# Optimization experiments

Hardware: AMD Instinct MI355X
Metric: run time of the kernel (lower is better)

The kernel has to match this reference:

```python
import jax, jax.numpy as jnp
import numpy as np

B = 512            # num graphs
NPG = 128          # nodes per graph (== output_dim; required by masked_fill broadcast)
N = B * NPG        # 65536 total nodes
EPG = 1024         # edges per graph
E = B * EPG        # 524288 edges
IN_D, HID_D, OUT_D = 128, 128, 128
EPS = 1e-5         # BatchNorm1d default eps
NEG = -10000000000.0


def setup_inputs() -> dict:
    key = jax.random.key(0)
    k = jax.random.split(key, 16)
    x = jax.random.normal(k[0], (N, IN_D), dtype=jnp.float32)
    # intra-graph random edges (PyG Batch never has cross-graph edges)
    g = jnp.repeat(jnp.arange(B, dtype=jnp.int32), EPG)
    src = g * NPG + jax.random.randint(k[1], (E,), 0, NPG, dtype=jnp.int32)
    dst = g * NPG + jax.random.randint(k[2], (E,), 0, NPG, dtype=jnp.int32)
    edge_index = jnp.stack([src, dst])  # [2, E]
    batch = jnp.repeat(jnp.arange(B, dtype=jnp.int32), NPG)  # [N]

    def lin(kk, fi, fo):
        s = 1.0 / np.sqrt(fi)
        return jax.random.uniform(kk, (fi, fo), jnp.float32, -s, s)

    W1 = lin(k[3], IN_D, HID_D); b1 = jnp.zeros((HID_D,), jnp.float32)
    W2 = lin(k[4], HID_D, HID_D); b2 = jnp.zeros((HID_D,), jnp.float32)
    W3 = lin(k[5], HID_D, OUT_D); b3 = jnp.zeros((OUT_D,), jnp.float32)
    gamma1 = jnp.ones((HID_D,), jnp.float32); beta1 = jnp.zeros((HID_D,), jnp.float32)
    gamma2 = jnp.ones((HID_D,), jnp.float32); beta2 = jnp.zeros((HID_D,), jnp.float32)
    rm1 = 0.1 * jax.random.normal(k[6], (HID_D,), jnp.float32)
    rv1 = jax.random.uniform(k[7], (HID_D,), jnp.float32, 0.5, 1.5)
    rm2 = 0.1 * jax.random.normal(k[8], (HID_D,), jnp.float32)
    rv2 = jax.random.uniform(k[9], (HID_D,), jnp.float32, 0.5, 1.5)
    return dict(x=x, edge_index=edge_index, batch=batch,
                W1=W1, b1=b1, gamma1=gamma1, beta1=beta1, rm1=rm1, rv1=rv1,
                W2=W2, b2=b2, gamma2=gamma2, beta2=beta2, rm2=rm2, rv2=rv2,
                W3=W3, b3=b3)


def reference(x, edge_index, batch, W1, b1, gamma1, beta1, rm1, rv1,
              W2, b2, gamma2, beta2, rm2, rv2, W3, b3):
    src, dst = edge_index[0], edge_index[1]
    loops = jnp.arange(N, dtype=src.dtype)
    fs = jnp.concatenate([src, loops])  # sources with self-loops
    fd = jnp.concatenate([dst, loops])  # targets with self-loops
    deg = jax.ops.segment_sum(jnp.ones_like(fd, jnp.float32), fd, num_segments=N)
    dis = jnp.where(deg > 0, jax.lax.rsqrt(deg), 0.0)
    norm = dis[fs] * dis[fd]  # D^-1/2 A_hat D^-1/2 per edge

    def gcn(h, W, b):
        h = h @ W
        msg = h[fs] * norm[:, None]            # [E+N, d] gather
        return jax.ops.segment_sum(msg, fd, num_segments=N) + b  # scatter-add

    def bn(h, g, bt, rm, rv):  # BatchNorm1d in eval mode (running stats)
        return (h - rm) * jax.lax.rsqrt(rv + EPS) * g + bt

    h = jax.nn.relu(bn(gcn(x, W1, b1), gamma1, beta1, rm1, rv1))
    # dropout is a no-op in eval mode
    h = jax.nn.relu(bn(gcn(h, W2, b2), gamma2, beta2, rm2, rv2))
    h = gcn(h, W3, b3)

    # global mean pool (all graphs have exactly NPG nodes)
    pooled = jax.ops.segment_sum(h, batch, num_segments=B) / NPG  # [B, OUT_D]

    # vectorized get_visited_nodes_and_update_embeddings:
    # a node is 'connected' if it appears as src or dst of an edge of its graph;
    # the minimum connected node index of each graph is exempted.
    connected = jnp.zeros((N,), bool).at[src].set(True).at[dst].set(True)
    ids = jnp.arange(N, dtype=jnp.int32)
    cand = jnp.where(connected, ids, N)
    min_pg = jax.ops.segment_min(cand, batch, num_segments=B)  # [B]
    mask = connected & (ids != min_pg[batch])                  # [N]
    return jnp.where(mask.reshape(B, NPG), NEG, pooled)
```

## Files before the change

### kernel.cpp

```cpp
#include <hip/hip_runtime.h>
#include <hip/hip_bf16.h>


#define NGRAPH 512
#define EPG 1024
#define NEDGE (NGRAPH * EPG)
#define NEGV -10000000000.0f
#define LDS_MAIN 62468

typedef float f32x16 __attribute__((ext_vector_type(16)));
typedef float f32x4  __attribute__((ext_vector_type(4)));

#define MFMA8(a, b, c) __builtin_amdgcn_mfma_f32_32x32x16_fp8_fp8(a, b, c, 0, 0, 0)

__device__ unsigned char g_wf[32768];

__device__ __forceinline__ unsigned swz8(unsigned row, unsigned byte_in_row) {
  return ((row << 7) + byte_in_row) ^ ((row & 15u) << 3);
}

__device__ __forceinline__ unsigned pk4(float a, float b, float c, float d) {
  int r = __builtin_amdgcn_cvt_pk_fp8_f32(a, b, 0, false);
  r = __builtin_amdgcn_cvt_pk_fp8_f32(c, d, r, true);
  return (unsigned)r;
}

__global__ void prep_w(const float* __restrict__ W1, const float* __restrict__ W2) {
  int gid = blockIdx.x * 256 + threadIdx.x;
  int lyr = gid >> 11, r = gid & 2047;
  int lane = r & 63, ks = (r >> 6) & 7, nt = r >> 9;
  const float* W = lyr ? W2 : W1;
  int fo = nt * 32 + (lane & 31);
  int k0 = ks * 16 + (lane >> 5) * 8;
  uint2 o;
  o.x = pk4(W[(k0 + 0) * 128 + fo], W[(k0 + 1) * 128 + fo],
            W[(k0 + 2) * 128 + fo], W[(k0 + 3) * 128 + fo]);
  o.y = pk4(W[(k0 + 4) * 128 + fo], W[(k0 + 5) * 128 + fo],
            W[(k0 + 6) * 128 + fo], W[(k0 + 7) * 128 + fo]);
  ((uint2*)g_wf)[gid] = o;
}

__global__ __launch_bounds__(512, 4) void gcn_all(
    const float* __restrict__ x, const int* __restrict__ ei,
    const float* __restrict__ b1v, const float* __restrict__ g1v,
    const float* __restrict__ be1v, const float* __restrict__ rm1v,
    const float* __restrict__ rv1v,
    const float* __restrict__ b2v, const float* __restrict__ g2v,
    const float* __restrict__ be2v, const float* __restrict__ rm2v,
    const float* __restrict__ rv2v,
    const float* __restrict__ W3g, const float* __restrict__ b3v,
    float* __restrict__ out) {
  extern __shared__ char sm[];
  char* AnB = sm;
  char* Y0  = sm + 16384;
  char* X0  = sm + 32768;
  unsigned* cntW  = (unsigned*)(sm + 49152);
  float*    dis   = (float*)(sm + 57344);
  unsigned* deg   = (unsigned*)(sm + 57856);
  unsigned* conn  = (unsigned*)(sm + 58368);
  float*    csumE = (float*)(sm + 58880);
  float*    scl1  = (float*)(sm + 59392);
  float*    shf1  = (float*)(sm + 59904);
  float*    scl2  = (float*)(sm + 60416);
  float*    shf2  = (float*)(sm + 60928);
  float*    vred  = (float*)(sm + 61440);
  int*      minid = (int*)(sm + 62464);

  const int tid = threadIdx.x;
  const int g   = blockIdx.x;
  const int lane = tid & 63;
  const int wid  = tid >> 6;
  const int l31  = lane & 31;
  const int hi   = lane >> 5;
  const int mt   = wid >> 1;
  const int nt0  = (wid & 1) * 2;

  const f32x4* xg = (const f32x4*)(x + (size_t)g * 128 * 128);
  f32x4 xr[8];
#pragma unroll
  for (int j = 0; j < 8; ++j) xr[j] = xg[tid + 512 * j];
  int es[2], ed[2];
#pragma unroll
  for (int j = 0; j < 2; ++j) {
    int e = g * EPG + tid + 512 * j;
    es[j] = ei[e] & 127;
    ed[j] = ei[NEDGE + e] & 127;
  }
  long wb0[8], wb1[8];
#pragma unroll
  for (int ks = 0; ks < 8; ++ks) {
    wb0[ks] = *(const long*)(g_wf + (nt0 + 0) * 4096 + ks * 512 + lane * 8);
    wb1[ks] = *(const long*)(g_wf + (nt0 + 1) * 4096 + ks * 512 + lane * 8);
  }

  {
    uint4 z; z.x = 0; z.y = 0; z.z = 0; z.w = 0;
    ((uint4*)cntW)[tid] = z;
  }
  if (tid < 128) {
    deg[tid] = 1u; conn[tid] = 0u; csumE[tid] = 0.f; vred[tid] = 0.f;
    float s1 = rsqrtf(rv1v[tid] + 1e-5f) * g1v[tid];
    scl1[tid] = s1;
    shf1[tid] = be1v[tid] + (b1v[tid] - rm1v[tid]) * s1;
    float s2 = rsqrtf(rv2v[tid] + 1e-5f) * g2v[tid];
    scl2[tid] = s2;
    shf2[tid] = be2v[tid] + (b2v[tid] - rm2v[tid]) * s2;
  }
  if (tid == 0) *minid = 128;
  __syncthreads();

#pragma unroll
  for (int j = 0; j < 2; ++j) {
    atomicAdd(&cntW[ed[j] * 16 + (es[j] >> 3)], 1u << (4 * (es[j] & 7)));
    atomicAdd(&deg[ed[j]], 1u);
    conn[es[j]] = 1u;
    conn[ed[j]] = 1u;
  }
#pragma unroll
  for (int j = 0; j < 8; ++j) {
    int k = tid + 512 * j;
    *(unsigned*)(Y0 + swz8(k >> 5, (k & 31) * 4)) =
        pk4(xr[j][0], xr[j][1], xr[j][2], xr[j][3]);
  }
  __syncthreads();

  {
    int dr = tid >> 4;
    int q8 = tid & 15;
    int s0 = q8 * 8;
    uint4 dg0 = *(const uint4*)(deg + s0);
    uint4 dg1 = *(const uint4*)(deg + s0 + 4);
    float ds8[8] = {rsqrtf((float)dg0.x), rsqrtf((float)dg0.y),
                    rsqrtf((float)dg0.z), rsqrtf((float)dg0.w),
                    rsqrtf((float)dg1.x), rsqrtf((float)dg1.y),
                    rsqrtf((float)dg1.z), rsqrtf((float)dg1.w)};
#pragma unroll
    for (int rr = 0; rr < 4; ++rr) {
      int row = dr + 32 * rr;
      float dd = rsqrtf((float)deg[row]);
      unsigned w = cntW[row * 16 + q8];
      float v[8];
#pragma unroll
      for (int i = 0; i < 8; ++i)
        v[i] = (float)((w >> (4 * i)) & 15u) * dd * ds8[i];
      if (row >= s0 && row < s0 + 8) v[row - s0] += dd * dd;
      uint2 o;
      o.x = pk4(v[0], v[1], v[2], v[3]);
      o.y = pk4(v[4], v[5], v[6], v[7]);
      *(uint2*)(AnB + swz8(row, s0)) = o;
    }
  }
#pragma unroll
  for (int j = 0; j < 2; ++j)
    atomicAdd(&csumE[es[j]],
              rsqrtf((float)deg[es[j]]) * rsqrtf((float)deg[ed[j]]));
  if (tid < 128) {
    dis[tid] = rsqrtf((float)deg[tid]);
    if (conn[tid]) atomicMin(minid, tid);
  }
  {
    long af[8];
#pragma unroll
    for (int ks = 0; ks < 8; ++ks)
      af[ks] = *(const long*)(Y0 + swz8(mt * 32 + l31, ks * 16 + hi * 8));
    f32x16 c0 = {}, c1 = {};
#pragma unroll
    for (int ks = 0; ks < 8; ++ks) {
      c0 = MFMA8(af[ks], wb0[ks], c0);
      c1 = MFMA8(af[ks], wb1[ks], c1);
    }
#pragma unroll
    for (int n = 0; n < 2; ++n) {
      int f = (nt0 + n) * 32 + l31;
      const f32x16& c = n ? c1 : c0;
#pragma unroll
      for (int q = 0; q < 4; ++q)
        *(unsigned*)(X0 + swz8(f, mt * 32 + q * 8 + hi * 4)) =
            pk4(c[q * 4 + 0], c[q * 4 + 1], c[q * 4 + 2], c[q * 4 + 3]);
    }
  }
  __syncthreads();

  {
    long af[8], b0[8], b1[8];
#pragma unroll
    for (int ks = 0; ks < 8; ++ks) {
      af[ks] = *(const long*)(X0 + swz8(mt * 32 + l31, ks * 16 + hi * 8));
      b0[ks] = *(const long*)(AnB + swz8((nt0 + 0) * 32 + l31, ks * 16 + hi * 8));
      b1[ks] = *(const long*)(AnB + swz8((nt0 + 1) * 32 + l31, ks * 16 + hi * 8));
    }
    f32x16 c0 = {}, c1 = {};
#pragma unroll
    for (int ks = 0; ks < 8; ++ks) {
      c0 = MFMA8(af[ks], b0[ks], c0);
      c1 = MFMA8(af[ks], b1[ks], c1);
    }
#pragma unroll
    for (int n = 0; n < 2; ++n) {
      int d = (nt0 + n) * 32 + l31;
      const f32x16& c = n ? c1 : c0;
#pragma unroll
      for (int q = 0; q < 4; ++q) {
        int f0 = mt * 32 + q * 8 + hi * 4;
        f32x4 s4 = *(const f32x4*)(scl1 + f0);
        f32x4 h4 = *(const f32x4*)(shf1 + f0);
        *(unsigned*)(Y0 + swz8(d, f0)) =
            pk4(fmaxf(c[q * 4 + 0] * s4[0] + h4[0], 0.f),
                fmaxf(c[q * 4 + 1] * s4[1] + h4[1], 0.f),
                fmaxf(c[q * 4 + 2] * s4[2] + h4[2], 0.f),
                fmaxf(c[q * 4 + 3] * s4[3] + h4[3], 0.f));
      }
    }
  }
  __syncthreads();

  {
    long w20[8], w21[8];
#pragma unroll
    for (int ks = 0; ks < 8; ++ks) {
      w20[ks] = *(const long*)(g_wf + 16384 + (nt0 + 0) * 4096 + ks * 512 + lane * 8);
      w21[ks] = *(const long*)(g_wf + 16384 + (nt0 + 1) * 4096 + ks * 512 + lane * 8);
    }
    long af[8];
#pragma unroll
    for (int ks = 0; ks < 8; ++ks)
      af[ks] = *(const long*)(Y0 + swz8(mt * 32 + l31, ks * 16 + hi * 8));
    f32x16 c0 = {}, c1 = {};
#pragma unroll
    for (int ks = 0; ks < 8; ++ks) {
      c0 = MFMA8(af[ks], w20[ks], c0);
      c1 = MFMA8(af[ks], w21[ks], c1);
    }
#pragma unroll
    for (int n = 0; n < 2; ++n) {
      int f = (nt0 + n) * 32 + l31;
      const f32x16& c = n ? c1 : c0;
#pragma unroll
      for (int q = 0; q < 4; ++q)
        *(unsigned*)(X0 + swz8(f, mt * 32 + q * 8 + hi * 4)) =
            pk4(c[q * 4 + 0], c[q * 4 + 1], c[q * 4 + 2], c[q * 4 + 3]);
    }
  }
  __syncthreads();

  {
    long af[8], b0[8], b1[8];
#pragma unroll
    for (int ks = 0; ks < 8; ++ks) {
      af[ks] = *(const long*)(X0 + swz8(mt * 32 + l31, ks * 16 + hi * 8));
      b0[ks] = *(const long*)(AnB + swz8((nt0 + 0) * 32 + l31, ks * 16 + hi * 8));
      b1[ks] = *(const long*)(AnB + swz8((nt0 + 1) * 32 + l31, ks * 16 + hi * 8));
    }
    f32x16 c0 = {}, c1 = {};
#pragma unroll
    for (int ks = 0; ks < 8; ++ks) {
      c0 = MFMA8(af[ks], b0[ks], c0);
      c1 = MFMA8(af[ks], b1[ks], c1);
    }
    int nA = (nt0 + 0) * 32 + l31, nB = (nt0 + 1) * 32 + l31;
    float dvA = dis[nA], dvB = dis[nB];
    float csA = csumE[nA] + dvA * dvA;
    float csB = csumE[nB] + dvB * dvB;
#pragma unroll
    for (int q = 0; q < 4; ++q) {
      int f0 = mt * 32 + q * 8 + hi * 4;
      f32x4 s4 = *(const f32x4*)(scl2 + f0);
      f32x4 h4 = *(const f32x4*)(shf2 + f0);
#pragma unroll
      for (int j = 0; j < 4; ++j) {
        float s = csA * fmaxf(c0[q * 4 + j] * s4[j] + h4[j], 0.f) +
                  csB * fmaxf(c1[q * 4 + j] * s4[j] + h4[j], 0.f);
        s += __shfl_xor(s, 1, 32);
        s += __shfl_xor(s, 2, 32);
        s += __shfl_xor(s, 4, 32);
        s += __shfl_xor(s, 8, 32);
        s += __shfl_xor(s, 16, 32);
        if (l31 == 0) atomicAdd(&vred[f0 + j], s);
      }
    }
  }
  __syncthreads();

  if (tid < 128) {
    float acc = 0.f;
#pragma unroll 8
    for (int f4 = 0; f4 < 32; ++f4) {
      f32x4 vr = *(const f32x4*)(vred + f4 * 4);
      acc += vr[0] * W3g[(f4 * 4 + 0) * 128 + tid];
      acc += vr[1] * W3g[(f4 * 4 + 1) * 128 + tid];
      acc += vr[2] * W3g[(f4 * 4 + 2) * 128 + tid];
      acc += vr[3] * W3g[(f4 * 4 + 3) * 128 + tid];
    }
    bool msk = (conn[tid] != 0u) && (tid != *minid);
    float val = acc * (1.0f / 128.0f) + b3v[tid];
    out[(size_t)g * 128 + tid] = msk ? NEGV : val;
  }
}

extern "C" void kernel_launch(void* const* d_in, const int* in_sizes, int n_in,
                              void* d_out, int out_size, void* d_ws, size_t ws_size,
                              hipStream_t stream) {
  (void)in_sizes; (void)n_in; (void)out_size; (void)d_ws; (void)ws_size;
  const float* x   = (const float*)d_in[0];
  const int*   ei  = (const int*)d_in[1];
  const float* W1  = (const float*)d_in[3];
  const float* b1  = (const float*)d_in[4];
  const float* g1  = (const float*)d_in[5];
  const float* be1 = (const float*)d_in[6];
  const float* rm1 = (const float*)d_in[7];
  const float* rv1 = (const float*)d_in[8];
  const float* W2  = (const float*)d_in[9];
  const float* b2  = (const float*)d_in[10];
  const float* g2  = (const float*)d_in[11];
  const float* be2 = (const float*)d_in[12];
  const float* rm2 = (const float*)d_in[13];
  const float* rv2 = (const float*)d_in[14];
  const float* W3  = (const float*)d_in[15];
  const float* b3  = (const float*)d_in[16];

  prep_w<<<dim3(16), dim3(256), 0, stream>>>(W1, W2);
  gcn_all<<<dim3(NGRAPH), dim3(512), LDS_MAIN, stream>>>(
      x, ei, b1, g1, be1, rm1, rv1, b2, g2, be2, rm2, rv2, W3, b3,
      (float*)d_out);
}
```

Measured before the change: 31.47 us.

## Process two graphs per workgroup to amortize weight loads and barriers

```diff
diff --git a/kernel.cpp b/kernel.cpp
--- a/kernel.cpp
+++ b/kernel.cpp
@@ -6,7 +6,8 @@
 #define EPG 1024
 #define NEDGE (NGRAPH * EPG)
 #define NEGV -10000000000.0f
-#define LDS_MAIN 62468
+#define GSTRIDE 62720
+#define LDS_MAIN (2 * GSTRIDE)
 
 typedef float f32x16 __attribute__((ext_vector_type(16)));
 typedef float f32x4  __attribute__((ext_vector_type(4)));
@@ -40,7 +41,7 @@
   ((uint2*)g_wf)[gid] = o;
 }
 
-__global__ __launch_bounds__(512, 4) void gcn_all(
+__global__ __launch_bounds__(512, 2) void gcn_all2(
     const float* __restrict__ x, const int* __restrict__ ei,
     const float* __restrict__ b1v, const float* __restrict__ g1v,
     const float* __restrict__ be1v, const float* __restrict__ rm1v,
@@ -51,23 +52,13 @@
     const float* __restrict__ W3g, const float* __restrict__ b3v,
     float* __restrict__ out) {
   extern __shared__ char sm[];
-  char* AnB = sm;
-  char* Y0  = sm + 16384;
-  char* X0  = sm + 32768;
-  unsigned* cntW  = (unsigned*)(sm + 49152);
-  float*    dis   = (float*)(sm + 57344);
-  unsigned* deg   = (unsigned*)(sm + 57856);
-  unsigned* conn  = (unsigned*)(sm + 58368);
-  float*    csumE = (float*)(sm + 58880);
-  float*    scl1  = (float*)(sm + 59392);
-  float*    shf1  = (float*)(sm + 59904);
-  float*    scl2  = (float*)(sm + 60416);
-  float*    shf2  = (float*)(sm + 60928);
-  float*    vred  = (float*)(sm + 61440);
-  int*      minid = (int*)(sm + 62464);
+  float* scl1 = (float*)(sm + 60416);
+  float* shf1 = (float*)(sm + 60928);
+  float* scl2 = (float*)(sm + 61440);
+  float* shf2 = (float*)(sm + 61952);
 
   const int tid = threadIdx.x;
-  const int g   = blockIdx.x;
+  const int g0  = blockIdx.x * 2;
   const int lane = tid & 63;
   const int wid  = tid >> 6;
   const int l31  = lane & 31;
@@ -75,17 +66,22 @@
   const int mt   = wid >> 1;
   const int nt0  = (wid & 1) * 2;
 
-  const f32x4* xg = (const f32x4*)(x + (size_t)g * 128 * 128);
-  f32x4 xr[8];
-#pragma unroll
-  for (int j = 0; j < 8; ++j) xr[j] = xg[tid + 512 * j];
-  int es[2], ed[2];
-#pragma unroll
-  for (int j = 0; j < 2; ++j) {
-    int e = g * EPG + tid + 512 * j;
-    es[j] = ei[e] & 127;
-    ed[j] = ei[NEDGE + e] & 127;
-  }
+  f32x4 xr[2][8];
+#pragma unroll
+  for (int gg = 0; gg < 2; ++gg) {
+    const f32x4* xg = (const f32x4*)(x + (size_t)(g0 + gg) * 16384);
+#pragma unroll
+    for (int j = 0; j < 8; ++j) xr[gg][j] = xg[tid + 512 * j];
+  }
+  int es[2][2], ed[2][2];
+#pragma unroll
+  for (int gg = 0; gg < 2; ++gg)
+#pragma unroll
+    for (int j = 0; j < 2; ++j) {
+      int e = (g0 + gg) * EPG + tid + 512 * j;
+      es[gg][j] = ei[e] & 127;
+      ed[gg][j] = ei[NEDGE + e] & 127;
+    }
   long wb0[8], wb1[8];
 #pragma unroll
   for (int ks = 0; ks < 8; ++ks) {
@@ -95,10 +91,22 @@
 
   {
     uint4 z; z.x = 0; z.y = 0; z.z = 0; z.w = 0;
-    ((uint4*)cntW)[tid] = z;
+#pragma unroll
+    for (int gg = 0; gg < 2; ++gg)
+      ((uint4*)(sm + gg * GSTRIDE + 49152))[tid] = z;
+  }
+#pragma unroll
+  for (int gg = 0; gg < 2; ++gg) {
+    char* blk = sm + gg * GSTRIDE;
+    if (tid < 128) {
+      ((unsigned*)(blk + 57856))[tid] = 1u;
+      ((unsigned*)(blk + 58368))[tid] = 0u;
+      ((float*)(blk + 58880))[tid] = 0.f;
+      ((float*)(blk + 59392))[tid] = 0.f;
+    }
+    if (tid == 0) *(int*)(blk + 59904) = 128;
   }
   if (tid < 128) {
-    deg[tid] = 1u; conn[tid] = 0u; csumE[tid] = 0.f; vred[tid] = 0.f;
     float s1 = rsqrtf(rv1v[tid] + 1e-5f) * g1v[tid];
     scl1[tid] = s1;
     shf1[tid] = be1v[tid] + (b1v[tid] - rm1v[tid]) * s1;
@@ -106,82 +114,108 @@
     scl2[tid] = s2;
     shf2[tid] = be2v[tid] + (b2v[tid] - rm2v[tid]) * s2;
   }
-  if (tid == 0) *minid = 128;
-  __syncthreads();
-
-#pragma unroll
-  for (int j = 0; j < 2; ++j) {
-    atomicAdd(&cntW[ed[j] * 16 + (es[j] >> 3)], 1u << (4 * (es[j] & 7)));
-    atomicAdd(&deg[ed[j]], 1u);
-    conn[es[j]] = 1u;
-    conn[ed[j]] = 1u;
-  }
-#pragma unroll
-  for (int j = 0; j < 8; ++j) {
-    int k = tid + 512 * j;
-    *(unsigned*)(Y0 + swz8(k >> 5, (k & 31) * 4)) =
-        pk4(xr[j][0], xr[j][1], xr[j][2], xr[j][3]);
-  }
-  __syncthreads();
-
-  {
-    int dr = tid >> 4;
-    int q8 = tid & 15;
-    int s0 = q8 * 8;
-    uint4 dg0 = *(const uint4*)(deg + s0);
-    uint4 dg1 = *(const uint4*)(deg + s0 + 4);
-    float ds8[8] = {rsqrtf((float)dg0.x), rsqrtf((float)dg0.y),
-                    rsqrtf((float)dg0.z), rsqrtf((float)dg0.w),
-                    rsqrtf((float)dg1.x), rsqrtf((float)dg1.y),
-                    rsqrtf((float)dg1.z), rsqrtf((float)dg1.w)};
-#pragma unroll
-    for (int rr = 0; rr < 4; ++rr) {
-      int row = dr + 32 * rr;
-      float dd = rsqrtf((float)deg[row]);
-      unsigned w = cntW[row * 16 + q8];
-      float v[8];
-#pragma unroll
-      for (int i = 0; i < 8; ++i)
-        v[i] = (float)((w >> (4 * i)) & 15u) * dd * ds8[i];
-      if (row >= s0 && row < s0 + 8) v[row - s0] += dd * dd;
-      uint2 o;
-      o.x = pk4(v[0], v[1], v[2], v[3]);
-      o.y = pk4(v[4], v[5], v[6], v[7]);
-      *(uint2*)(AnB + swz8(row, s0)) = o;
-    }
-  }
-#pragma unroll
-  for (int j = 0; j < 2; ++j)
-    atomicAdd(&csumE[es[j]],
-              rsqrtf((float)deg[es[j]]) * rsqrtf((float)deg[ed[j]]));
-  if (tid < 128) {
-    dis[tid] = rsqrtf((float)deg[tid]);
-    if (conn[tid]) atomicMin(minid, tid);
-  }
-  {
-    long af[8];
-#pragma unroll
-    for (int ks = 0; ks < 8; ++ks)
-      af[ks] = *(const long*)(Y0 + swz8(mt * 32 + l31, ks * 16 + hi * 8));
-    f32x16 c0 = {}, c1 = {};
-#pragma unroll
-    for (int ks = 0; ks < 8; ++ks) {
-      c0 = MFMA8(af[ks], wb0[ks], c0);
-      c1 = MFMA8(af[ks], wb1[ks], c1);
-    }
-#pragma unroll
-    for (int n = 0; n < 2; ++n) {
-      int f = (nt0 + n) * 32 + l31;
-      const f32x16& c = n ? c1 : c0;
-#pragma unroll
-      for (int q = 0; q < 4; ++q)
-        *(unsigned*)(X0 + swz8(f, mt * 32 + q * 8 + hi * 4)) =
-            pk4(c[q * 4 + 0], c[q * 4 + 1], c[q * 4 + 2], c[q * 4 + 3]);
-    }
-  }
-  __syncthreads();
-
-  {
+  __syncthreads();
+
+#pragma unroll
+  for (int gg = 0; gg < 2; ++gg) {
+    char* blk = sm + gg * GSTRIDE;
+    unsigned* cntW = (unsigned*)(blk + 49152);
+    unsigned* deg  = (unsigned*)(blk + 57856);
+    unsigned* conn = (unsigned*)(blk + 58368);
+#pragma unroll
+    for (int j = 0; j < 2; ++j) {
+      atomicAdd(&cntW[ed[gg][j] * 16 + (es[gg][j] >> 3)],
+                1u << (4 * (es[gg][j] & 7)));
+      atomicAdd(&deg[ed[gg][j]], 1u);
+      conn[es[gg][j]] = 1u;
+      conn[ed[gg][j]] = 1u;
+    }
+    char* Y0 = blk + 16384;
+#pragma unroll
+    for (int j = 0; j < 8; ++j) {
+      int k = tid + 512 * j;
+      *(unsigned*)(Y0 + swz8(k >> 5, (k & 31) * 4)) =
+          pk4(xr[gg][j][0], xr[gg][j][1], xr[gg][j][2], xr[gg][j][3]);
+    }
+  }
+  __syncthreads();
+
+#pragma unroll
+  for (int gg = 0; gg < 2; ++gg) {
+    char* blk = sm + gg * GSTRIDE;
+    char* AnB = blk;
+    char* Y0  = blk + 16384;
+    char* X0  = blk + 32768;
+    unsigned* cntW  = (unsigned*)(blk + 49152);
+    float*    dis   = (float*)(blk + 57344);
+    unsigned* deg   = (unsigned*)(blk + 57856);
+    unsigned* conn  = (unsigned*)(blk + 58368);
+    float*    csumE = (float*)(blk + 58880);
+    int*      minid = (int*)(blk + 59904);
+    {
+      int dr = tid >> 4;
+      int q8 = tid & 15;
+      int s0 = q8 * 8;
+      uint4 dg0 = *(const uint4*)(deg + s0);
+      uint4 dg1 = *(const uint4*)(deg + s0 + 4);
+      float ds8[8] = {rsqrtf((float)dg0.x), rsqrtf((float)dg0.y),
+                      rsqrtf((float)dg0.z), rsqrtf((float)dg0.w),
+                      rsqrtf((float)dg1.x), rsqrtf((float)dg1.y),
+                      rsqrtf((float)dg1.z), rsqrtf((float)dg1.w)};
+#pragma unroll
+      for (int rr = 0; rr < 4; ++rr) {
+        int row = dr + 32 * rr;
+        float dd = rsqrtf((float)deg[row]);
+        unsigned w = cntW[row * 16 + q8];
+        float v[8];
+#pragma unroll
+        for (int i = 0; i < 8; ++i)
+          v[i] = (float)((w >> (4 * i)) & 15u) * dd * ds8[i];
+        if (row >= s0 && row < s0 + 8) v[row - s0] += dd * dd;
+        uint2 o;
+        o.x = pk4(v[0], v[1], v[2], v[3]);
+        o.y = pk4(v[4], v[5], v[6], v[7]);
+        *(uint2*)(AnB + swz8(row, s0)) = o;
+      }
+    }
+#pragma unroll
+    for (int j = 0; j < 2; ++j)
+      atomicAdd(&csumE[es[gg][j]],
+                rsqrtf((float)deg[es[gg][j]]) * rsqrtf((float)deg[ed[gg][j]]));
+    if (tid < 128) {
+      dis[tid] = rsqrtf((float)deg[tid]);
+      if (conn[tid]) atomicMin(minid, tid);
+    }
+    {
+      long af[8];
+#pragma unroll
+      for (int ks = 0; ks < 8; ++ks)
+        af[ks] = *(const long*)(Y0 + swz8(mt * 32 + l31, ks * 16 + hi * 8));
+      f32x16 c0 = {}, c1 = {};
+#pragma unroll
+      for (int ks = 0; ks < 8; ++ks) {
+        c0 = MFMA8(af[ks], wb0[ks], c0);
+        c1 = MFMA8(af[ks], wb1[ks], c1);
+      }
+#pragma unroll
+      for (int n = 0; n < 2; ++n) {
+        int f = (nt0 + n) * 32 + l31;
+        const f32x16& c = n ? c1 : c0;
+#pragma unroll
+        for (int q = 0; q < 4; ++q)
+          *(unsigned*)(X0 + swz8(f, mt * 32 + q * 8 + hi * 4)) =
+              pk4(c[q * 4 + 0], c[q * 4 + 1], c[q * 4 + 2], c[q * 4 + 3]);
+      }
+    }
+  }
+  __syncthreads();
+
+#pragma unroll
+  for (int gg = 0; gg < 2; ++gg) {
+    char* blk = sm + gg * GSTRIDE;
+    char* AnB = blk;
+    char* Y0  = blk + 16384;
+    char* X0  = blk + 32768;
     long af[8], b0[8], b1[8];
 #pragma unroll
     for (int ks = 0; ks < 8; ++ks) {
@@ -221,29 +255,42 @@
       w20[ks] = *(const long*)(g_wf + 16384 + (nt0 + 0) * 4096 + ks * 512 + lane * 8);
       w21[ks] = *(const long*)(g_wf + 16384 + (nt0 + 1) * 4096 + ks * 512 + lane * 8);
     }
-    long af[8];
-#pragma unroll
-    for (int ks = 0; ks < 8; ++ks)
-      af[ks] = *(const long*)(Y0 + swz8(mt * 32 + l31, ks * 16 + hi * 8));
-    f32x16 c0 = {}, c1 = {};
-#pragma unroll
-    for (int ks = 0; ks < 8; ++ks) {
-      c0 = MFMA8(af[ks], w20[ks], c0);
-      c1 = MFMA8(af[ks], w21[ks], c1);
-    }
-#pragma unroll
-    for (int n = 0; n < 2; ++n) {
-      int f = (nt0 + n) * 32 + l31;
-      const f32x16& c = n ? c1 : c0;
-#pragma unroll
-      for (int q = 0; q < 4; ++q)
-        *(unsigned*)(X0 + swz8(f, mt * 32 + q * 8 + hi * 4)) =
-            pk4(c[q * 4 + 0], c[q * 4 + 1], c[q * 4 + 2], c[q * 4 + 3]);
-    }
-  }
-  __syncthreads();
-
-  {
+#pragma unroll
+    for (int gg = 0; gg < 2; ++gg) {
+      char* blk = sm + gg * GSTRIDE;
+      char* Y0  = blk + 16384;
+      char* X0  = blk + 32768;
+      long af[8];
+#pragma unroll
+      for (int ks = 0; ks < 8; ++ks)
+        af[ks] = *(const long*)(Y0 + swz8(mt * 32 + l31, ks * 16 + hi * 8));
+      f32x16 c0 = {}, c1 = {};
+#pragma unroll
+      for (int ks = 0; ks < 8; ++ks) {
+        c0 = MFMA8(af[ks], w20[ks], c0);
+        c1 = MFMA8(af[ks], w21[ks], c1);
+      }
+#pragma unroll
+      for (int n = 0; n < 2; ++n) {
+        int f = (nt0 + n) * 32 + l31;
+        const f32x16& c = n ? c1 : c0;
+#pragma unroll
+        for (int q = 0; q < 4; ++q)
+          *(unsigned*)(X0 + swz8(f, mt * 32 + q * 8 + hi * 4)) =
+              pk4(c[q * 4 + 0], c[q * 4 + 1], c[q * 4 + 2], c[q * 4 + 3]);
+      }
+    }
+  }
+  __syncthreads();
+
+#pragma unroll
+  for (int gg = 0; gg < 2; ++gg) {
+    char* blk = sm + gg * GSTRIDE;
+    char* AnB = blk;
+    char* X0  = blk + 32768;
+    float* dis   = (float*)(blk + 57344);
+    float* csumE = (float*)(blk + 58880);
+    float* vred  = (float*)(blk + 59392);
     long af[8], b0[8], b1[8];
 #pragma unroll
     for (int ks = 0; ks < 8; ++ks) {
@@ -281,19 +328,24 @@
   }
   __syncthreads();
 
-  if (tid < 128) {
+  if (tid < 256) {
+    int gg = tid >> 7, n = tid & 127;
+    char* blk = sm + gg * GSTRIDE;
+    float*    vred  = (float*)(blk + 59392);
+    unsigned* conn  = (unsigned*)(blk + 58368);
+    int*      minid = (int*)(blk + 59904);
     float acc = 0.f;
 #pragma unroll 8
     for (int f4 = 0; f4 < 32; ++f4) {
       f32x4 vr = *(const f32x4*)(vred + f4 * 4);
-      acc += vr[0] * W3g[(f4 * 4 + 0) * 128 + tid];
-      acc += vr[1] * W3g[(f4 * 4 + 1) * 128 + tid];
-      acc += vr[2] * W3g[(f4 * 4 + 2) * 128 + tid];
-      acc += vr[3] * W3g[(f4 * 4 + 3) * 128 + tid];
-    }
-    bool msk = (conn[tid] != 0u) && (tid != *minid);
-    float val = acc * (1.0f / 128.0f) + b3v[tid];
-    out[(size_t)g * 128 + tid] = msk ? NEGV : val;
+      acc += vr[0] * W3g[(f4 * 4 + 0) * 128 + n];
+      acc += vr[1] * W3g[(f4 * 4 + 1) * 128 + n];
+      acc += vr[2] * W3g[(f4 * 4 + 2) * 128 + n];
+      acc += vr[3] * W3g[(f4 * 4 + 3) * 128 + n];
+    }
+    bool msk = (conn[n] != 0u) && (n != *minid);
+    float val = acc * (1.0f / 128.0f) + b3v[n];
+    out[(size_t)(g0 + gg) * 128 + n] = msk ? NEGV : val;
   }
 }
 
@@ -318,8 +370,11 @@
   const float* W3  = (const float*)d_in[15];
   const float* b3  = (const float*)d_in[16];
 
+  (void)hipFuncSetAttribute((const void*)gcn_all2,
+                            hipFuncAttributeMaxDynamicSharedMemorySize,
+                            LDS_MAIN);
   prep_w<<<dim3(16), dim3(256), 0, stream>>>(W1, W2);
-  gcn_all<<<dim3(NGRAPH), dim3(512), LDS_MAIN, stream>>>(
+  gcn_all2<<<dim3(NGRAPH / 2), dim3(512), LDS_MAIN, stream>>>(
       x, ei, b1, g1, be1, rm1, rv1, b2, g2, be2, rm2, rv2, W3, b3,
       (float*)d_out);
 }
```

Result: slower. 39.07 us (+24.1%).
